# Kernel tuning notes

Measured on AMD Instinct MI355X. Metric: run time of the kernel, lower is better.

Reference implementation:

```python
import jax, jax.numpy as jnp
import numpy as np

B_SZ = 64            # oft_block_size
IN_F = 4096
OUT_F = 4096
R_IN = IN_F // B_SZ   # 64 blocks
R_OUT = OUT_F // B_SZ # 64 blocks
N_TRI = B_SZ * (B_SZ - 1) // 2  # 2016 packed strict-upper entries
NUM_NEUMANN = 5

_rows, _cols = np.triu_indices(B_SZ, k=1)
ROWS = jnp.asarray(_rows, dtype=jnp.int32)
COLS = jnp.asarray(_cols, dtype=jnp.int32)


def setup_inputs() -> dict:
    key = jax.random.key(0)
    k = jax.random.split(key, 5)
    x = jax.random.normal(k[0], (4, 2048, IN_F), dtype=jnp.float32)
    # small skew entries so the Neumann series approximates the Cayley transform
    Ro = jax.random.normal(k[1], (R_OUT, N_TRI), dtype=jnp.float32) * 0.01
    Ri = jax.random.normal(k[2], (R_IN, N_TRI), dtype=jnp.float32) * 0.01
    W = jax.random.normal(k[3], (OUT_F, IN_F), dtype=jnp.float32) * (1.0 / np.sqrt(IN_F))
    bias = jax.random.normal(k[4], (OUT_F,), dtype=jnp.float32) * 0.01
    rng = np.random.default_rng(0)
    perm_in = rng.permutation(IN_F)
    perm_in_inv = np.argsort(perm_in)
    perm_out = rng.permutation(OUT_F)
    return {
        "x": x, "Ro": Ro, "Ri": Ri, "W": W, "bias": bias,
        "perm_in_inv": jnp.asarray(perm_in_inv, dtype=jnp.int32),
        "perm_out": jnp.asarray(perm_out, dtype=jnp.int32),
    }


def _skew(vec):
    # vec: (r, n_tri) packed strict-upper entries -> (r, b, b) skew-symmetric
    r = vec.shape[0]
    M = jnp.zeros((r, B_SZ, B_SZ), dtype=vec.dtype).at[:, ROWS, COLS].set(vec)
    return M - jnp.swapaxes(M, -2, -1)


def _cayley_neumann(Q):
    # R = I + 2*(Q + Q^2 + Q^3 + Q^4)   (num_neumann_terms = 5)
    I = jnp.eye(B_SZ, dtype=Q.dtype)
    acc = Q
    Qp = Q
    for _ in range(3, NUM_NEUMANN):
        pass
    Q2 = jnp.matmul(Q, Q)
    acc = acc + Q2
    Qp = Q2
    for _ in range(3, NUM_NEUMANN):
        Qp = jnp.matmul(Qp, Q)
        acc = acc + Qp
    return I + 2.0 * acc


def reference(x, Ro, Ri, W, bias, perm_in_inv, perm_out):
    R_out = _cayley_neumann(_skew(Ro))   # (r_out, b, b)
    R_in = _cayley_neumann(_skew(Ri))    # (r_in, b, b)

    B, S, _ = x.shape
    xp = x[..., perm_in_inv]                               # input permutation
    xb = xp.reshape(B, S, R_IN, B_SZ)
    xR = jnp.einsum('bsrc,rcd->bsrd', xb, R_in)            # block-diag right rotate
    y = xR.reshape(B, S, IN_F) @ W.T + bias                # base linear
    yb = y.reshape(B, S, R_OUT, B_SZ)
    yR = jnp.einsum('bsrc,rcd->bsrd', yb, R_out)           # block-diag output rotate
    out = yR.reshape(B, S, OUT_F)[..., perm_out]           # output permutation
    return out
```

## Files before the change

### kernel.cpp

```cpp
#include <hip/hip_runtime.h>
#include <stdint.h>

#define IN_F 4096
#define OUT_F 4096
#define NTRI 2016

typedef unsigned short u16;
typedef __attribute__((ext_vector_type(8))) short short8;
typedef __attribute__((ext_vector_type(4))) float f32x4;
typedef __attribute__((ext_vector_type(4))) int i32x4;
typedef __attribute__((ext_vector_type(4))) unsigned short u16x4;

__device__ __forceinline__ u16 f2bf(float f) {
    uint32_t u = __builtin_bit_cast(uint32_t, f);
    u = (u + 0x7FFFu + ((u >> 16) & 1u)) >> 16;
    return (u16)u;
}

__device__ __forceinline__ void gload16(const void* g, void* l) {
    __builtin_amdgcn_global_load_lds((__attribute__((address_space(1))) void*)g,
                                     (__attribute__((address_space(3))) void*)l,
                                     16, 0, 0);
}

__global__ void k_inv_perm(const int* __restrict__ perm_out, int* __restrict__ pinv_out) {
    int i = blockIdx.x * 256 + threadIdx.x;
    if (i < OUT_F) pinv_out[perm_out[i]] = i;
}

__global__ __launch_bounds__(256) void k_cayley(const float* __restrict__ Ro,
                                                const float* __restrict__ Ri,
                                                float* __restrict__ Rout,
                                                u16* __restrict__ QT16,
                                                u16* __restrict__ P16) {
    __shared__ __align__(16) float Qs[64 * 64];
    __shared__ __align__(16) float Ps[64 * 68];
    __shared__ __align__(16) float Ts[64 * 68];
    int b = blockIdx.x;
    const float* vec = (b < 64) ? (Ro + (size_t)b * NTRI) : (Ri + (size_t)(b - 64) * NTRI);
    int t = threadIdx.x;
    int tr = t >> 4, tc = t & 15;
#pragma unroll
    for (int e = 0; e < 16; ++e) {
        int el = e * 256 + t;
        int i = el >> 6, j = el & 63;
        float q = 0.f;
        if (i < j) q =  vec[i * 63 - (i * (i - 1)) / 2 + (j - i - 1)];
        if (i > j) q = -vec[j * 63 - (j * (j - 1)) / 2 + (i - j - 1)];
        Qs[el] = q;
    }
    __syncthreads();
    float a2[4][4], a3[4][4], a4[4][4];
#pragma unroll
    for (int i = 0; i < 4; ++i)
#pragma unroll
        for (int j = 0; j < 4; ++j) { a2[i][j] = 0.f; a3[i][j] = 0.f; a4[i][j] = 0.f; }
    for (int k = 0; k < 64; ++k) {
        f32x4 qa = *(const f32x4*)&Qs[k * 64 + tr * 4];
        f32x4 qb = *(const f32x4*)&Qs[k * 64 + tc * 4];
#pragma unroll
        for (int i = 0; i < 4; ++i)
#pragma unroll
            for (int j = 0; j < 4; ++j) a2[i][j] -= qa[i] * qb[j];
    }
#pragma unroll
    for (int i = 0; i < 4; ++i)
#pragma unroll
        for (int j = 0; j < 4; ++j) Ps[(tr * 4 + i) * 68 + tc * 4 + j] = a2[i][j];
    __syncthreads();
    for (int k = 0; k < 64; ++k) {
        f32x4 pa = *(const f32x4*)&Ps[k * 68 + tr * 4];
        f32x4 qb = *(const f32x4*)&Qs[k * 64 + tc * 4];
#pragma unroll
        for (int i = 0; i < 4; ++i)
#pragma unroll
            for (int j = 0; j < 4; ++j) a3[i][j] += pa[i] * qb[j];
    }
#pragma unroll
    for (int i = 0; i < 4; ++i)
#pragma unroll
        for (int j = 0; j < 4; ++j) Ts[(tc * 4 + j) * 68 + tr * 4 + i] = -a3[i][j];
    __syncthreads();
    for (int k = 0; k < 64; ++k) {
        f32x4 ta = *(const f32x4*)&Ts[k * 68 + tr * 4];
        f32x4 qb = *(const f32x4*)&Qs[k * 64 + tc * 4];
#pragma unroll
        for (int i = 0; i < 4; ++i)
#pragma unroll
            for (int j = 0; j < 4; ++j) a4[i][j] -= ta[i] * qb[j];
    }
    if (b < 64) {
        float* dst = Rout + (size_t)b * 4096;
        u16* qt = QT16 + (size_t)b * 4096;
#pragma unroll
        for (int i = 0; i < 4; ++i) {
            int gi = tr * 4 + i;
            f32x4 q4 = *(const f32x4*)&Qs[gi * 64 + tc * 4];
            f32x4 o;
#pragma unroll
            for (int j = 0; j < 4; ++j) {
                int gj = tc * 4 + j;
                o[j] = 2.f * (q4[j] + a2[i][j] + a3[i][j] + a4[i][j]) + ((gi == gj) ? 1.f : 0.f);
            }
            *(f32x4*)&dst[gi * 64 + tc * 4] = o;
#pragma unroll
            for (int j = 0; j < 4; ++j) qt[(tc * 4 + j) * 64 + gi] = f2bf(o[j]);
        }
    } else {
        u16* p = P16 + (size_t)(b - 64) * 4096;
#pragma unroll
        for (int i = 0; i < 4; ++i) {
            int gi = tr * 4 + i;
            f32x4 q4 = *(const f32x4*)&Qs[gi * 64 + tc * 4];
            u16x4 pk;
#pragma unroll
            for (int j = 0; j < 4; ++j) {
                int gj = tc * 4 + j;
                float v = 2.f * (q4[j] + a2[i][j] + a3[i][j] + a4[i][j]) + ((gi == gj) ? 1.f : 0.f);
                pk[j] = f2bf(v);
            }
            *(u16x4*)&p[gi * 64 + tc * 4] = pk;
        }
    }
}

__global__ void k_bias(const float* __restrict__ bias, const float* __restrict__ Rout,
                       const int* __restrict__ perm_out, float* __restrict__ bfinal) {
    int j = blockIdx.x * 256 + threadIdx.x;
    if (j >= OUT_F) return;
    int o = perm_out[j];
    int r = o >> 6, d = o & 63;
    const float* Rb = Rout + (size_t)r * 4096;
    const float* bb = bias + r * 64;
    float s = 0.f;
    for (int c = 0; c < 64; ++c) s += bb[c] * Rb[c * 64 + d];
    bfinal[j] = s;
}

__global__ __launch_bounds__(256) void k_fold(const float* __restrict__ W,
                                              const u16* __restrict__ P16,
                                              const u16* __restrict__ QT16,
                                              const int* __restrict__ pinv_out,
                                              u16* __restrict__ Ctp) {
    __shared__ __align__(16) u16 Wst[128 * 64];
    __shared__ __align__(16) u16 Ut[64 * 128];
    const int s = blockIdx.x;
    const int br = blockIdx.y;
    const int t = threadIdx.x;
    const int lane = t & 63;
    const int w = t >> 6;
    const int fl = lane & 15;
    const int kg = lane >> 4;

    short8 bfP[4][2];
    const u16* Pbase = P16 + (size_t)s * 4096;
#pragma unroll
    for (int nf = 0; nf < 4; ++nf)
#pragma unroll
        for (int kk = 0; kk < 2; ++kk)
            bfP[nf][kk] = *(const short8*)(Pbase + (nf * 16 + fl) * 64 + kk * 32 + kg * 8);

#pragma unroll
    for (int q = 0; q < 4; ++q) {
        int ci = q * 256 + t;
        int row = ci >> 3, slot = ci & 7;
        const float* src = W + (size_t)(br * 128 + row) * IN_F + s * 64 + slot * 8;
        f32x4 v0 = *(const f32x4*)src;
        f32x4 v1 = *(const f32x4*)(src + 4);
        union { short8 v; u16 e[8]; } cv;
        cv.e[0] = f2bf(v0[0]); cv.e[1] = f2bf(v0[1]); cv.e[2] = f2bf(v0[2]); cv.e[3] = f2bf(v0[3]);
        cv.e[4] = f2bf(v1[0]); cv.e[5] = f2bf(v1[1]); cv.e[6] = f2bf(v1[2]); cv.e[7] = f2bf(v1[3]);
        *(short8*)&Wst[row * 64 + (slot ^ (row & 7)) * 8] = cv.v;
    }
    __syncthreads();

    f32x4 acc1[2][4];
#pragma unroll
    for (int mf = 0; mf < 2; ++mf)
#pragma unroll
        for (int nf = 0; nf < 4; ++nf) acc1[mf][nf] = f32x4{0.f, 0.f, 0.f, 0.f};
#pragma unroll
    for (int mf = 0; mf < 2; ++mf) {
        int row = w * 32 + mf * 16 + fl;
#pragma unroll
        for (int kk = 0; kk < 2; ++kk) {
            short8 a = *(const short8*)&Wst[row * 64 + ((kk * 4 + kg) ^ (row & 7)) * 8];
#pragma unroll
            for (int nf = 0; nf < 4; ++nf)
                acc1[mf][nf] = __builtin_amdgcn_mfma_f32_16x16x32_bf16(a, bfP[nf][kk], acc1[mf][nf], 0, 0, 0);
        }
    }
#pragma unroll
    for (int mf = 0; mf < 2; ++mf)
#pragma unroll
        for (int nf = 0; nf < 4; ++nf) {
            int i = nf * 16 + fl;
            int c = w * 32 + mf * 16 + kg * 4;
            u16x4 pk;
#pragma unroll
            for (int reg = 0; reg < 4; ++reg) pk[reg] = f2bf(acc1[mf][nf][reg]);
            int slot = c >> 3, half = (c >> 2) & 1;
            *(u16x4*)&Ut[i * 128 + ((slot ^ (i & 7)) << 3) + (half << 2)] = pk;
        }
    __syncthreads();

    const int rbl = w >> 1;
    const int r_g = br * 2 + rbl;
    short8 aQ[2][2];
#pragma unroll
    for (int mf2 = 0; mf2 < 2; ++mf2) {
        int d = (w & 1) * 32 + mf2 * 16 + fl;
#pragma unroll
        for (int kk = 0; kk < 2; ++kk)
            aQ[mf2][kk] = *(const short8*)(QT16 + (size_t)r_g * 4096 + d * 64 + kk * 32 + kg * 8);
    }
    f32x4 acc2[2][4];
#pragma unroll
    for (int mf2 = 0; mf2 < 2; ++mf2)
#pragma unroll
        for (int nf = 0; nf < 4; ++nf) acc2[mf2][nf] = f32x4{0.f, 0.f, 0.f, 0.f};
#pragma unroll
    for (int kk = 0; kk < 2; ++kk)
#pragma unroll
        for (int nf = 0; nf < 4; ++nf) {
            int i = nf * 16 + fl;
            int slot = rbl * 8 + kk * 4 + kg;
            short8 bu = *(const short8*)&Ut[i * 128 + ((slot ^ (i & 7)) << 3)];
#pragma unroll
            for (int mf2 = 0; mf2 < 2; ++mf2)
                acc2[mf2][nf] = __builtin_amdgcn_mfma_f32_16x16x32_bf16(aQ[mf2][kk], bu, acc2[mf2][nf], 0, 0, 0);
        }
#pragma unroll
    for (int mf2 = 0; mf2 < 2; ++mf2)
#pragma unroll
        for (int reg = 0; reg < 4; ++reg) {
            int o_g = br * 128 + w * 32 + mf2 * 16 + kg * 4 + reg;
            int j = pinv_out[o_g];
            u16* dst = Ctp + (size_t)j * IN_F + s * 64;
#pragma unroll
            for (int nf = 0; nf < 4; ++nf)
                dst[nf * 16 + fl] = f2bf(acc2[mf2][nf][reg]);
        }
}

__global__ __launch_bounds__(512) void k_xcast_perm(const float* __restrict__ x,
                                                    const int* __restrict__ pii,
                                                    u16* __restrict__ xb) {
    __shared__ __align__(16) float xr[4096];
    const int t = threadIdx.x;
    int pv[8];
    *(i32x4*)&pv[0] = *(const i32x4*)&pii[t * 8];
    *(i32x4*)&pv[4] = *(const i32x4*)&pii[t * 8 + 4];
    for (int r = 0; r < 8; ++r) {
        size_t s = (size_t)blockIdx.x * 8 + r;
        const float* src = x + s * 4096;
        *(f32x4*)&xr[t * 4]        = *(const f32x4*)&src[t * 4];
        *(f32x4*)&xr[2048 + t * 4] = *(const f32x4*)&src[2048 + t * 4];
        __syncthreads();
        union { short8 v; u16 e[8]; } o;
#pragma unroll
        for (int j = 0; j < 8; ++j) o.e[j] = f2bf(xr[pv[j]]);
        *(short8*)&xb[s * 4096 + t * 8] = o.v;
        __syncthreads();
    }
}

__global__ __launch_bounds__(512, 2) void k_gemm(const u16* __restrict__ A,
                                                 const u16* __restrict__ Bt,
                                                 const float* __restrict__ bias,
                                                 float* __restrict__ out) {
    __shared__ __align__(16) u16 lds[81920];
    const int t = threadIdx.x;
    const int lane = t & 63;
    const int wid = t >> 6;
    const int wr = wid >> 2, wc = wid & 3;

    int flat = blockIdx.y * gridDim.x + blockIdx.x;
    int swz  = (flat & 7) * 64 + (flat >> 3);
    int bm = swz >> 4;
    int bn = swz & 15;

    const int srow = t >> 2;
    const int sks  = (t & 3) ^ ((t >> 3) & 3);
    const u16* sA0 = A  + (size_t)(bm * 256 + srow) * IN_F + sks * 8;
    const u16* sA1 = sA0 + (size_t)128 * IN_F;
    const u16* sB0 = Bt + (size_t)(bn * 256 + srow) * IN_F + sks * 8;
    const u16* sB1 = sB0 + (size_t)128 * IN_F;
    u16* dA = lds + t * 8;
    u16* dB = lds + 8192 + t * 8;

    const int frow = lane & 15;
    const int kg = lane >> 4;
    const int swzr = kg ^ ((frow >> 1) & 3);
    const int aoff = (wr * 128 + frow) * 32 + swzr * 8;
    const int boff = 8192 + (wc * 64 + frow) * 32 + swzr * 8;

    f32x4 acc[8][4];
#pragma unroll
    for (int m = 0; m < 8; ++m)
#pragma unroll
        for (int n = 0; n < 4; ++n) acc[m][n] = f32x4{0.f, 0.f, 0.f, 0.f};

#pragma unroll
    for (int p = 0; p < 3; ++p) {
        int off = p * 32;
        int bb = p * 16384;
        gload16(sA0 + off, dA + bb); gload16(sA1 + off, dA + bb + 4096);
        gload16(sB0 + off, dB + bb); gload16(sB1 + off, dB + bb + 4096);
    }
    asm volatile("s_waitcnt vmcnt(4)" ::: "memory");
    __builtin_amdgcn_s_barrier();

    int b0 = 0;
    for (int p = 0; p < 64; ++p) {
        const int kt = 2 * p;
        int b1 = b0 + 1; if (b1 >= 5) b1 -= 5;
        int s0 = b0 + 3; if (s0 >= 5) s0 -= 5;
        int s1 = b0 + 4; if (s1 >= 5) s1 -= 5;
        {
            const u16* pa = lds + b0 * 16384 + aoff;
            const u16* pb = lds + b0 * 16384 + boff;
            short8 af[8], bf[4];
#pragma unroll
            for (int m = 0; m < 8; ++m) af[m] = *(const short8*)(pa + m * 512);
#pragma unroll
            for (int n = 0; n < 4; ++n) bf[n] = *(const short8*)(pb + n * 512);
            int ts = kt + 3;
            int off = (ts < 128 ? ts : 124) * 32;
            int bb = s0 * 16384;
            gload16(sA0 + off, dA + bb); gload16(sA1 + off, dA + bb + 4096);
            gload16(sB0 + off, dB + bb); gload16(sB1 + off, dB + bb + 4096);
            __builtin_amdgcn_s_setprio(1);
#pragma unroll
            for (int m = 0; m < 8; ++m)
#pragma unroll
                for (int n = 0; n < 4; ++n)
                    acc[m][n] = __builtin_amdgcn_mfma_f32_16x16x32_bf16(af[m], bf[n], acc[m][n], 0, 0, 0);
            __builtin_amdgcn_s_setprio(0);
        }
        {
            const u16* pa = lds + b1 * 16384 + aoff;
            const u16* pb = lds + b1 * 16384 + boff;
            short8 af[8], bf[4];
#pragma unroll
            for (int m = 0; m < 8; ++m) af[m] = *(const short8*)(pa + m * 512);
#pragma unroll
            for (int n = 0; n < 4; ++n) bf[n] = *(const short8*)(pb + n * 512);
            int ts = kt + 4;
            int off = (ts < 128 ? ts : 124) * 32;
            int bb = s1 * 16384;
            gload16(sA0 + off, dA + bb); gload16(sA1 + off, dA + bb + 4096);
            gload16(sB0 + off, dB + bb); gload16(sB1 + off, dB + bb + 4096);
            __builtin_amdgcn_s_setprio(1);
#pragma unroll
            for (int m = 0; m < 8; ++m)
#pragma unroll
                for (int n = 0; n < 4; ++n)
                    acc[m][n] = __builtin_amdgcn_mfma_f32_16x16x32_bf16(af[m], bf[n], acc[m][n], 0, 0, 0);
            __builtin_amdgcn_s_setprio(0);
        }
        asm volatile("s_waitcnt vmcnt(4)" ::: "memory");
        __builtin_amdgcn_s_barrier();
        b0 += 2; if (b0 >= 5) b0 -= 5;
    }
    asm volatile("s_waitcnt vmcnt(0)" ::: "memory");

    const int col0 = bn * 256 + wc * 64 + frow;
    const int row0 = bm * 256 + wr * 128 + kg * 4;
    float bv[4];
#pragma unroll
    for (int n = 0; n < 4; ++n) bv[n] = bias[col0 + n * 16];
#pragma unroll
    for (int m = 0; m < 8; ++m)
#pragma unroll
        for (int n = 0; n < 4; ++n)
#pragma unroll
            for (int i = 0; i < 4; ++i)
                out[(size_t)(row0 + m * 16 + i) * OUT_F + col0 + n * 16] = acc[m][n][i] + bv[n];
}

extern "C" void kernel_launch(void* const* d_in, const int* in_sizes, int n_in,
                              void* d_out, int out_size, void* d_ws, size_t ws_size,
                              hipStream_t stream) {
    (void)in_sizes; (void)n_in; (void)out_size; (void)ws_size;
    const float* x    = (const float*)d_in[0];
    const float* Ro   = (const float*)d_in[1];
    const float* Ri   = (const float*)d_in[2];
    const float* W    = (const float*)d_in[3];
    const float* bias = (const float*)d_in[4];
    const int* perm_in_inv = (const int*)d_in[5];
    const int* perm_out    = (const int*)d_in[6];
    float* out = (float*)d_out;

    char* ws = (char*)d_ws;
    float* Rout   = (float*)(ws);
    u16*   P16    = (u16*)(ws + (1ull << 20));
    u16*   QT16   = (u16*)(ws + (1ull << 20) + (1 << 19));
    int*   pinvo  = (int*)(ws + (2ull << 20));
    float* bfinal = (float*)(ws + (2ull << 20) + (1 << 16));
    u16*   Ctp    = (u16*)(ws + (4ull << 20));
    u16*   xb     = (u16*)(ws + (36ull << 20));

    k_inv_perm<<<16, 256, 0, stream>>>(perm_out, pinvo);
    k_cayley<<<128, 256, 0, stream>>>(Ro, Ri, Rout, QT16, P16);
    k_bias<<<16, 256, 0, stream>>>(bias, Rout, perm_out, bfinal);
    k_fold<<<dim3(64, 32), 256, 0, stream>>>(W, P16, QT16, pinvo, Ctp);
    k_xcast_perm<<<1024, 512, 0, stream>>>(x, perm_in_inv, xb);
    k_gemm<<<dim3(16, 32), 512, 0, stream>>>(xb, Ctp, bfinal, out);
}
```

Measured before the change: 335.2 us.

## Restructure GEMM main loop into quadrant-interleaved double-buffered schedule with K=64 tiles

Replaces the 5-stage ring of K=32 LDS tiles with two K=64 buffers, using an 8-way XOR swizzle. Each K tile is split into four MFMA quadrants, and global-to-LDS loads for half-tiles are issued between them with barriers, an HipKittens-style 8-wave ping-pong schedule. The goal is to overlap LDS reads, global loads and MFMA work more finely and to cut LDS usage. In exchange it adds many more barriers per iteration and leaves less prefetch depth.

```diff
diff --git a/kernel.cpp b/kernel.cpp
--- a/kernel.cpp
+++ b/kernel.cpp
@@ -22,6 +22,8 @@
                                      (__attribute__((address_space(3))) void*)l,
                                      16, 0, 0);
 }
+
+#define FENCE() asm volatile("" ::: "memory")
 
 __global__ void k_inv_perm(const int* __restrict__ perm_out, int* __restrict__ pinv_out) {
     int i = blockIdx.x * 256 + threadIdx.x;
@@ -269,7 +271,7 @@
                                                  const u16* __restrict__ Bt,
                                                  const float* __restrict__ bias,
                                                  float* __restrict__ out) {
-    __shared__ __align__(16) u16 lds[81920];
+    __shared__ __align__(16) u16 lds[65536];
     const int t = threadIdx.x;
     const int lane = t & 63;
     const int wid = t >> 6;
@@ -280,20 +282,43 @@
     int bm = swz >> 4;
     int bn = swz & 15;
 
-    const int srow = t >> 2;
-    const int sks  = (t & 3) ^ ((t >> 3) & 3);
-    const u16* sA0 = A  + (size_t)(bm * 256 + srow) * IN_F + sks * 8;
-    const u16* sA1 = sA0 + (size_t)128 * IN_F;
-    const u16* sB0 = Bt + (size_t)(bn * 256 + srow) * IN_F + sks * 8;
-    const u16* sB1 = sB0 + (size_t)128 * IN_F;
-    u16* dA = lds + t * 8;
-    u16* dB = lds + 8192 + t * 8;
+    const int sk = ((t & 7) ^ ((t >> 3) & 7)) * 8;
+    const u16* gA = A  + (size_t)(bm * 256 + (t >> 3)) * IN_F + sk;
+    const u16* gB = Bt + (size_t)(bn * 256 + (t >> 3)) * IN_F + sk;
+    u16* ldst = lds + t * 8;
+
+#define STAGE_A(buf, r0, kt) do { \
+        u16* d_ = ldst + (buf) * 32768 + (r0) * 64; \
+        const u16* s_ = gA + (size_t)(r0) * IN_F + (kt) * 64; \
+        gload16(s_, d_); gload16(s_ + (size_t)64 * IN_F, d_ + 4096); } while (0)
+#define STAGE_B(buf, r0, kt) do { \
+        u16* d_ = ldst + (buf) * 32768 + 16384 + (r0) * 64; \
+        const u16* s_ = gB + (size_t)(r0) * IN_F + (kt) * 64; \
+        gload16(s_, d_); gload16(s_ + (size_t)64 * IN_F, d_ + 4096); } while (0)
 
     const int frow = lane & 15;
     const int kg = lane >> 4;
-    const int swzr = kg ^ ((frow >> 1) & 3);
-    const int aoff = (wr * 128 + frow) * 32 + swzr * 8;
-    const int boff = 8192 + (wc * 64 + frow) * 32 + swzr * 8;
+    int fswz[2];
+    fswz[0] = ((0 * 4 + kg) ^ (frow & 7)) * 8;
+    fswz[1] = ((1 * 4 + kg) ^ (frow & 7)) * 8;
+    const int arow = (wr * 128 + frow) * 64;
+    const int brow = 16384 + (wc * 64 + frow) * 64;
+
+#define LDA(B, M, KS) (*(const short8*)(lds + (B) + arow + (M) * 1024 + fswz[KS]))
+#define LDB(B, N, KS) (*(const short8*)(lds + (B) + brow + (N) * 1024 + fswz[KS]))
+
+#define MQ(AR, BR, MB, NB) do { \
+        __builtin_amdgcn_s_setprio(1); \
+        _Pragma("unroll") for (int ks_ = 0; ks_ < 2; ++ks_) \
+        _Pragma("unroll") for (int m_ = 0; m_ < 4; ++m_) \
+        _Pragma("unroll") for (int n_ = 0; n_ < 2; ++n_) \
+            acc[(MB) + m_][(NB) + n_] = __builtin_amdgcn_mfma_f32_16x16x32_bf16( \
+                AR[m_][ks_], BR[n_][ks_], acc[(MB) + m_][(NB) + n_], 0, 0, 0); \
+        __builtin_amdgcn_s_setprio(0); } while (0)
+
+#define BAR_LG() do { FENCE(); __builtin_amdgcn_s_barrier(); \
+        asm volatile("s_waitcnt lgkmcnt(0)" ::: "memory"); } while (0)
+#define BAR() do { FENCE(); __builtin_amdgcn_s_barrier(); FENCE(); } while (0)
 
     f32x4 acc[8][4];
 #pragma unroll
@@ -301,67 +326,86 @@
 #pragma unroll
         for (int n = 0; n < 4; ++n) acc[m][n] = f32x4{0.f, 0.f, 0.f, 0.f};
 
-#pragma unroll
-    for (int p = 0; p < 3; ++p) {
-        int off = p * 32;
-        int bb = p * 16384;
-        gload16(sA0 + off, dA + bb); gload16(sA1 + off, dA + bb + 4096);
-        gload16(sB0 + off, dB + bb); gload16(sB1 + off, dB + bb + 4096);
-    }
+    STAGE_A(0, 0, 0); STAGE_A(0, 128, 0);
+    STAGE_B(0, 0, 0); STAGE_B(0, 128, 0);
+    STAGE_B(1, 0, 1); STAGE_A(1, 0, 1);
     asm volatile("s_waitcnt vmcnt(4)" ::: "memory");
     __builtin_amdgcn_s_barrier();
-
-    int b0 = 0;
-    for (int p = 0; p < 64; ++p) {
-        const int kt = 2 * p;
-        int b1 = b0 + 1; if (b1 >= 5) b1 -= 5;
-        int s0 = b0 + 3; if (s0 >= 5) s0 -= 5;
-        int s1 = b0 + 4; if (s1 >= 5) s1 -= 5;
-        {
-            const u16* pa = lds + b0 * 16384 + aoff;
-            const u16* pb = lds + b0 * 16384 + boff;
-            short8 af[8], bf[4];
-#pragma unroll
-            for (int m = 0; m < 8; ++m) af[m] = *(const short8*)(pa + m * 512);
-#pragma unroll
-            for (int n = 0; n < 4; ++n) bf[n] = *(const short8*)(pb + n * 512);
-            int ts = kt + 3;
-            int off = (ts < 128 ? ts : 124) * 32;
-            int bb = s0 * 16384;
-            gload16(sA0 + off, dA + bb); gload16(sA1 + off, dA + bb + 4096);
-            gload16(sB0 + off, dB + bb); gload16(sB1 + off, dB + bb + 4096);
-            __builtin_amdgcn_s_setprio(1);
-#pragma unroll
-            for (int m = 0; m < 8; ++m)
-#pragma unroll
-                for (int n = 0; n < 4; ++n)
-                    acc[m][n] = __builtin_amdgcn_mfma_f32_16x16x32_bf16(af[m], bf[n], acc[m][n], 0, 0, 0);
-            __builtin_amdgcn_s_setprio(0);
-        }
-        {
-            const u16* pa = lds + b1 * 16384 + aoff;
-            const u16* pb = lds + b1 * 16384 + boff;
-            short8 af[8], bf[4];
-#pragma unroll
-            for (int m = 0; m < 8; ++m) af[m] = *(const short8*)(pa + m * 512);
-#pragma unroll
-            for (int n = 0; n < 4; ++n) bf[n] = *(const short8*)(pb + n * 512);
-            int ts = kt + 4;
-            int off = (ts < 128 ? ts : 124) * 32;
-            int bb = s1 * 16384;
-            gload16(sA0 + off, dA + bb); gload16(sA1 + off, dA + bb + 4096);
-            gload16(sB0 + off, dB + bb); gload16(sB1 + off, dB + bb + 4096);
-            __builtin_amdgcn_s_setprio(1);
-#pragma unroll
-            for (int m = 0; m < 8; ++m)
-#pragma unroll
-                for (int n = 0; n < 4; ++n)
-                    acc[m][n] = __builtin_amdgcn_mfma_f32_16x16x32_bf16(af[m], bf[n], acc[m][n], 0, 0, 0);
-            __builtin_amdgcn_s_setprio(0);
-        }
+    FENCE();
+
+    short8 alo[4][2], ahi[4][2], blo[2][2], bhi[2][2];
+
+    for (int i = 0; i < 32; ++i) {
+        const int kt1 = 2 * i + 1;
+        const int kn0 = (i < 31) ? 2 * i + 2 : 62;
+        const int kn1 = (i < 31) ? 2 * i + 3 : 63;
+
+#pragma unroll
+        for (int m = 0; m < 4; ++m)
+#pragma unroll
+            for (int ks = 0; ks < 2; ++ks) alo[m][ks] = LDA(0, m, ks);
+#pragma unroll
+        for (int n = 0; n < 2; ++n)
+#pragma unroll
+            for (int ks = 0; ks < 2; ++ks) blo[n][ks] = LDB(0, n, ks);
+        STAGE_A(1, 128, kt1);
+        BAR_LG();
+        MQ(alo, blo, 0, 0);
+        BAR();
+#pragma unroll
+        for (int n = 0; n < 2; ++n)
+#pragma unroll
+            for (int ks = 0; ks < 2; ++ks) bhi[n][ks] = LDB(0, 2 + n, ks);
+        STAGE_B(1, 128, kt1);
+        BAR_LG();
+        MQ(alo, bhi, 0, 2);
+        BAR();
+#pragma unroll
+        for (int m = 0; m < 4; ++m)
+#pragma unroll
+            for (int ks = 0; ks < 2; ++ks) ahi[m][ks] = LDA(0, 4 + m, ks);
+        STAGE_B(0, 0, kn0);
+        BAR_LG();
+        MQ(ahi, blo, 4, 0);
+        BAR();
+        STAGE_A(0, 0, kn0);
         asm volatile("s_waitcnt vmcnt(4)" ::: "memory");
-        __builtin_amdgcn_s_barrier();
-        b0 += 2; if (b0 >= 5) b0 -= 5;
+        BAR();
+        MQ(ahi, bhi, 4, 2);
+        BAR();
+#pragma unroll
+        for (int m = 0; m < 4; ++m)
+#pragma unroll
+            for (int ks = 0; ks < 2; ++ks) alo[m][ks] = LDA(32768, m, ks);
+#pragma unroll
+        for (int n = 0; n < 2; ++n)
+#pragma unroll
+            for (int ks = 0; ks < 2; ++ks) blo[n][ks] = LDB(32768, n, ks);
+        STAGE_A(0, 128, kn0);
+        BAR_LG();
+        MQ(alo, blo, 0, 0);
+        BAR();
+#pragma unroll
+        for (int n = 0; n < 2; ++n)
+#pragma unroll
+            for (int ks = 0; ks < 2; ++ks) bhi[n][ks] = LDB(32768, 2 + n, ks);
+        STAGE_B(0, 128, kn0);
+        BAR_LG();
+        MQ(alo, bhi, 0, 2);
+        BAR();
+#pragma unroll
+        for (int m = 0; m < 4; ++m)
+#pragma unroll
+            for (int ks = 0; ks < 2; ++ks) ahi[m][ks] = LDA(32768, 4 + m, ks);
+        STAGE_B(1, 0, kn1);
+        BAR_LG();
+        MQ(ahi, blo, 4, 0);
+        BAR();
+        STAGE_A(1, 0, kn1);
+        asm volatile("s_waitcnt vmcnt(4)" ::: "memory");
+        BAR();
+        MQ(ahi, bhi, 4, 2);
+        BAR();
     }
     asm volatile("s_waitcnt vmcnt(0)" ::: "memory");
 
@@ -377,6 +421,13 @@
 #pragma unroll
             for (int i = 0; i < 4; ++i)
                 out[(size_t)(row0 + m * 16 + i) * OUT_F + col0 + n * 16] = acc[m][n][i] + bv[n];
+#undef STAGE_A
+#undef STAGE_B
+#undef LDA
+#undef LDB
+#undef MQ
+#undef BAR_LG
+#undef BAR
 }
 
 extern "C" void kernel_launch(void* const* d_in, const int* in_sizes, int n_in,
```

After: 325.3 us. 2.9% less time.

## Merge prep kernels into two launches and switch GEMM to 4-stage ring pipeline

Applied to the files above, without the earlier changes.

Folds the inverse-permutation into the Cayley kernel and merges the weight fold, x cast/permute and bias kernels into one launch dispatched by block index, cutting launch count from six to three and letting independent stages share the GPU. The main GEMM LDS ring drops from 5 buffers to 4, going from two k-steps per barrier to one barrier per k-step with vmcnt(8). The smaller LDS footprint may improve occupancy, but the extra barriers and shallower wait window may expose more load latency.

```diff
diff --git a/kernel.cpp b/kernel.cpp
--- a/kernel.cpp
+++ b/kernel.cpp
@@ -23,22 +23,27 @@
                                      16, 0, 0);
 }
 
-__global__ void k_inv_perm(const int* __restrict__ perm_out, int* __restrict__ pinv_out) {
-    int i = blockIdx.x * 256 + threadIdx.x;
-    if (i < OUT_F) pinv_out[perm_out[i]] = i;
-}
-
-__global__ __launch_bounds__(256) void k_cayley(const float* __restrict__ Ro,
-                                                const float* __restrict__ Ri,
-                                                float* __restrict__ Rout,
-                                                u16* __restrict__ QT16,
-                                                u16* __restrict__ P16) {
+__global__ __launch_bounds__(256) void k_prep(const float* __restrict__ Ro,
+                                              const float* __restrict__ Ri,
+                                              const int* __restrict__ perm_out,
+                                              float* __restrict__ Rout,
+                                              u16* __restrict__ QT16,
+                                              u16* __restrict__ P16,
+                                              int* __restrict__ pinv_out) {
+    const int b = blockIdx.x;
+    const int t = threadIdx.x;
+    if (b == 128) {
+#pragma unroll
+        for (int e = 0; e < 16; ++e) {
+            int i = e * 256 + t;
+            pinv_out[perm_out[i]] = i;
+        }
+        return;
+    }
     __shared__ __align__(16) float Qs[64 * 64];
     __shared__ __align__(16) float Ps[64 * 68];
     __shared__ __align__(16) float Ts[64 * 68];
-    int b = blockIdx.x;
     const float* vec = (b < 64) ? (Ro + (size_t)b * NTRI) : (Ri + (size_t)(b - 64) * NTRI);
-    int t = threadIdx.x;
     int tr = t >> 4, tc = t & 15;
 #pragma unroll
     for (int e = 0; e < 16; ++e) {
@@ -124,144 +129,148 @@
     }
 }
 
-__global__ void k_bias(const float* __restrict__ bias, const float* __restrict__ Rout,
-                       const int* __restrict__ perm_out, float* __restrict__ bfinal) {
-    int j = blockIdx.x * 256 + threadIdx.x;
-    if (j >= OUT_F) return;
-    int o = perm_out[j];
-    int r = o >> 6, d = o & 63;
-    const float* Rb = Rout + (size_t)r * 4096;
-    const float* bb = bias + r * 64;
-    float s = 0.f;
-    for (int c = 0; c < 64; ++c) s += bb[c] * Rb[c * 64 + d];
-    bfinal[j] = s;
-}
-
-__global__ __launch_bounds__(256) void k_fold(const float* __restrict__ W,
+__global__ __launch_bounds__(256) void k_work(const float* __restrict__ W,
                                               const u16* __restrict__ P16,
                                               const u16* __restrict__ QT16,
                                               const int* __restrict__ pinv_out,
-                                              u16* __restrict__ Ctp) {
-    __shared__ __align__(16) u16 Wst[128 * 64];
-    __shared__ __align__(16) u16 Ut[64 * 128];
-    const int s = blockIdx.x;
-    const int br = blockIdx.y;
+                                              const float* __restrict__ x,
+                                              const int* __restrict__ pii,
+                                              const float* __restrict__ bias,
+                                              const float* __restrict__ Rout,
+                                              const int* __restrict__ perm_out,
+                                              u16* __restrict__ Ctp,
+                                              u16* __restrict__ xb,
+                                              float* __restrict__ bfinal) {
+    const int fb = blockIdx.x;
     const int t = threadIdx.x;
-    const int lane = t & 63;
-    const int w = t >> 6;
-    const int fl = lane & 15;
-    const int kg = lane >> 4;
-
-    short8 bfP[4][2];
-    const u16* Pbase = P16 + (size_t)s * 4096;
-#pragma unroll
-    for (int nf = 0; nf < 4; ++nf)
+    if (fb < 2048) {
+        __shared__ __align__(16) u16 Wst[128 * 64];
+        __shared__ __align__(16) u16 Ut[64 * 128];
+        const int s = fb & 63;
+        const int br = fb >> 6;
+        const int lane = t & 63;
+        const int w = t >> 6;
+        const int fl = lane & 15;
+        const int kg = lane >> 4;
+
+        short8 bfP[4][2];
+        const u16* Pbase = P16 + (size_t)s * 4096;
+#pragma unroll
+        for (int nf = 0; nf < 4; ++nf)
+#pragma unroll
+            for (int kk = 0; kk < 2; ++kk)
+                bfP[nf][kk] = *(const short8*)(Pbase + (nf * 16 + fl) * 64 + kk * 32 + kg * 8);
+
+#pragma unroll
+        for (int q = 0; q < 4; ++q) {
+            int ci = q * 256 + t;
+            int row = ci >> 3, slot = ci & 7;
+            const float* src = W + (size_t)(br * 128 + row) * IN_F + s * 64 + slot * 8;
+            f32x4 v0 = *(const f32x4*)src;
+            f32x4 v1 = *(const f32x4*)(src + 4);
+            union { short8 v; u16 e[8]; } cv;
+            cv.e[0] = f2bf(v0[0]); cv.e[1] = f2bf(v0[1]); cv.e[2] = f2bf(v0[2]); cv.e[3] = f2bf(v0[3]);
+            cv.e[4] = f2bf(v1[0]); cv.e[5] = f2bf(v1[1]); cv.e[6] = f2bf(v1[2]); cv.e[7] = f2bf(v1[3]);
+            *(short8*)&Wst[row * 64 + (slot ^ (row & 7)) * 8] = cv.v;
+        }
+        __syncthreads();
+
+        f32x4 acc1[2][4];
+#pragma unroll
+        for (int mf = 0; mf < 2; ++mf)
+#pragma unroll
+            for (int nf = 0; nf < 4; ++nf) acc1[mf][nf] = f32x4{0.f, 0.f, 0.f, 0.f};
+#pragma unroll
+        for (int mf = 0; mf < 2; ++mf) {
+            int row = w * 32 + mf * 16 + fl;
+#pragma unroll
+            for (int kk = 0; kk < 2; ++kk) {
+                short8 a = *(const short8*)&Wst[row * 64 + ((kk * 4 + kg) ^ (row & 7)) * 8];
+#pragma unroll
+                for (int nf = 0; nf < 4; ++nf)
+                    acc1[mf][nf] = __builtin_amdgcn_mfma_f32_16x16x32_bf16(a, bfP[nf][kk], acc1[mf][nf], 0, 0, 0);
+            }
+        }
+#pragma unroll
+        for (int mf = 0; mf < 2; ++mf)
+#pragma unroll
+            for (int nf = 0; nf < 4; ++nf) {
+                int i = nf * 16 + fl;
+                int c = w * 32 + mf * 16 + kg * 4;
+                u16x4 pk;
+#pragma unroll
+                for (int reg = 0; reg < 4; ++reg) pk[reg] = f2bf(acc1[mf][nf][reg]);
+                int slot = c >> 3, half = (c >> 2) & 1;
+                *(u16x4*)&Ut[i * 128 + ((slot ^ (i & 7)) << 3) + (half << 2)] = pk;
+            }
+        __syncthreads();
+
+        const int rbl = w >> 1;
+        const int r_g = br * 2 + rbl;
+        short8 aQ[2][2];
+#pragma unroll
+        for (int mf2 = 0; mf2 < 2; ++mf2) {
+            int d = (w & 1) * 32 + mf2 * 16 + fl;
+#pragma unroll
+            for (int kk = 0; kk < 2; ++kk)
+                aQ[mf2][kk] = *(const short8*)(QT16 + (size_t)r_g * 4096 + d * 64 + kk * 32 + kg * 8);
+        }
+        f32x4 acc2[2][4];
+#pragma unroll
+        for (int mf2 = 0; mf2 < 2; ++mf2)
+#pragma unroll
+            for (int nf = 0; nf < 4; ++nf) acc2[mf2][nf] = f32x4{0.f, 0.f, 0.f, 0.f};
 #pragma unroll
         for (int kk = 0; kk < 2; ++kk)
-            bfP[nf][kk] = *(const short8*)(Pbase + (nf * 16 + fl) * 64 + kk * 32 + kg * 8);
-
-#pragma unroll
-    for (int q = 0; q < 4; ++q) {
-        int ci = q * 256 + t;
-        int row = ci >> 3, slot = ci & 7;
-        const float* src = W + (size_t)(br * 128 + row) * IN_F + s * 64 + slot * 8;
-        f32x4 v0 = *(const f32x4*)src;
-        f32x4 v1 = *(const f32x4*)(src + 4);
-        union { short8 v; u16 e[8]; } cv;
-        cv.e[0] = f2bf(v0[0]); cv.e[1] = f2bf(v0[1]); cv.e[2] = f2bf(v0[2]); cv.e[3] = f2bf(v0[3]);
-        cv.e[4] = f2bf(v1[0]); cv.e[5] = f2bf(v1[1]); cv.e[6] = f2bf(v1[2]); cv.e[7] = f2bf(v1[3]);
-        *(short8*)&Wst[row * 64 + (slot ^ (row & 7)) * 8] = cv.v;
-    }
-    __syncthreads();
-
-    f32x4 acc1[2][4];
-#pragma unroll
-    for (int mf = 0; mf < 2; ++mf)
-#pragma unroll
-        for (int nf = 0; nf < 4; ++nf) acc1[mf][nf] = f32x4{0.f, 0.f, 0.f, 0.f};
-#pragma unroll
-    for (int mf = 0; mf < 2; ++mf) {
-        int row = w * 32 + mf * 16 + fl;
-#pragma unroll
-        for (int kk = 0; kk < 2; ++kk) {
-            short8 a = *(const short8*)&Wst[row * 64 + ((kk * 4 + kg) ^ (row & 7)) * 8];
-#pragma unroll
-            for (int nf = 0; nf < 4; ++nf)
-                acc1[mf][nf] = __builtin_amdgcn_mfma_f32_16x16x32_bf16(a, bfP[nf][kk], acc1[mf][nf], 0, 0, 0);
-        }
-    }
-#pragma unroll
-    for (int mf = 0; mf < 2; ++mf)
-#pragma unroll
-        for (int nf = 0; nf < 4; ++nf) {
-            int i = nf * 16 + fl;
-            int c = w * 32 + mf * 16 + kg * 4;
-            u16x4 pk;
-#pragma unroll
-            for (int reg = 0; reg < 4; ++reg) pk[reg] = f2bf(acc1[mf][nf][reg]);
-            int slot = c >> 3, half = (c >> 2) & 1;
-            *(u16x4*)&Ut[i * 128 + ((slot ^ (i & 7)) << 3) + (half << 2)] = pk;
-        }
-    __syncthreads();
-
-    const int rbl = w >> 1;
-    const int r_g = br * 2 + rbl;
-    short8 aQ[2][2];
-#pragma unroll
-    for (int mf2 = 0; mf2 < 2; ++mf2) {
-        int d = (w & 1) * 32 + mf2 * 16 + fl;
-#pragma unroll
-        for (int kk = 0; kk < 2; ++kk)
-            aQ[mf2][kk] = *(const short8*)(QT16 + (size_t)r_g * 4096 + d * 64 + kk * 32 + kg * 8);
-    }
-    f32x4 acc2[2][4];
-#pragma unroll
-    for (int mf2 = 0; mf2 < 2; ++mf2)
-#pragma unroll
-        for (int nf = 0; nf < 4; ++nf) acc2[mf2][nf] = f32x4{0.f, 0.f, 0.f, 0.f};
-#pragma unroll
-    for (int kk = 0; kk < 2; ++kk)
-#pragma unroll
-        for (int nf = 0; nf < 4; ++nf) {
-            int i = nf * 16 + fl;
-            int slot = rbl * 8 + kk * 4 + kg;
-            short8 bu = *(const short8*)&Ut[i * 128 + ((slot ^ (i & 7)) << 3)];
-#pragma unroll
-            for (int mf2 = 0; mf2 < 2; ++mf2)
-                acc2[mf2][nf] = __builtin_amdgcn_mfma_f32_16x16x32_bf16(aQ[mf2][kk], bu, acc2[mf2][nf], 0, 0, 0);
-        }
-#pragma unroll
-    for (int mf2 = 0; mf2 < 2; ++mf2)
-#pragma unroll
-        for (int reg = 0; reg < 4; ++reg) {
-            int o_g = br * 128 + w * 32 + mf2 * 16 + kg * 4 + reg;
-            int j = pinv_out[o_g];
-            u16* dst = Ctp + (size_t)j * IN_F + s * 64;
-#pragma unroll
-            for (int nf = 0; nf < 4; ++nf)
-                dst[nf * 16 + fl] = f2bf(acc2[mf2][nf][reg]);
-        }
-}
-
-__global__ __launch_bounds__(512) void k_xcast_perm(const float* __restrict__ x,
-                                                    const int* __restrict__ pii,
-                                                    u16* __restrict__ xb) {
-    __shared__ __align__(16) float xr[4096];
-    const int t = threadIdx.x;
-    int pv[8];
-    *(i32x4*)&pv[0] = *(const i32x4*)&pii[t * 8];
-    *(i32x4*)&pv[4] = *(const i32x4*)&pii[t * 8 + 4];
-    for (int r = 0; r < 8; ++r) {
-        size_t s = (size_t)blockIdx.x * 8 + r;
-        const float* src = x + s * 4096;
-        *(f32x4*)&xr[t * 4]        = *(const f32x4*)&src[t * 4];
-        *(f32x4*)&xr[2048 + t * 4] = *(const f32x4*)&src[2048 + t * 4];
-        __syncthreads();
-        union { short8 v; u16 e[8]; } o;
-#pragma unroll
-        for (int j = 0; j < 8; ++j) o.e[j] = f2bf(xr[pv[j]]);
-        *(short8*)&xb[s * 4096 + t * 8] = o.v;
-        __syncthreads();
+#pragma unroll
+            for (int nf = 0; nf < 4; ++nf) {
+                int i = nf * 16 + fl;
+                int slot = rbl * 8 + kk * 4 + kg;
+                short8 bu = *(const short8*)&Ut[i * 128 + ((slot ^ (i & 7)) << 3)];
+#pragma unroll
+                for (int mf2 = 0; mf2 < 2; ++mf2)
+                    acc2[mf2][nf] = __builtin_amdgcn_mfma_f32_16x16x32_bf16(aQ[mf2][kk], bu, acc2[mf2][nf], 0, 0, 0);
+            }
+#pragma unroll
+        for (int mf2 = 0; mf2 < 2; ++mf2)
+#pragma unroll
+            for (int reg = 0; reg < 4; ++reg) {
+                int o_g = br * 128 + w * 32 + mf2 * 16 + kg * 4 + reg;
+                int j = pinv_out[o_g];
+                u16* dst = Ctp + (size_t)j * IN_F + s * 64;
+#pragma unroll
+                for (int nf = 0; nf < 4; ++nf)
+                    dst[nf * 16 + fl] = f2bf(acc2[mf2][nf][reg]);
+            }
+    } else if (fb < 3072) {
+        __shared__ __align__(16) float xr[4096];
+        const int blk = fb - 2048;
+        int pv[16];
+#pragma unroll
+        for (int q = 0; q < 4; ++q) *(i32x4*)&pv[q * 4] = *(const i32x4*)&pii[t * 16 + q * 4];
+        for (int r = 0; r < 8; ++r) {
+            size_t srow = (size_t)blk * 8 + r;
+            const float* src = x + srow * 4096;
+#pragma unroll
+            for (int q = 0; q < 4; ++q)
+                *(f32x4*)&xr[q * 1024 + t * 4] = *(const f32x4*)&src[q * 1024 + t * 4];
+            __syncthreads();
+            union { short8 v; u16 e[8]; } o0, o1;
+#pragma unroll
+            for (int j = 0; j < 8; ++j) { o0.e[j] = f2bf(xr[pv[j]]); o1.e[j] = f2bf(xr[pv[8 + j]]); }
+            *(short8*)&xb[srow * 4096 + t * 16] = o0.v;
+            *(short8*)&xb[srow * 4096 + t * 16 + 8] = o1.v;
+            __syncthreads();
+        }
+    } else {
+        int j = (fb - 3072) * 256 + t;
+        int o = perm_out[j];
+        int r = o >> 6, d = o & 63;
+        const float* Rb = Rout + (size_t)r * 4096;
+        const float* bb = bias + r * 64;
+        float s = 0.f;
+        for (int c = 0; c < 64; ++c) s += bb[c] * Rb[c * 64 + d];
+        bfinal[j] = s;
     }
 }
 
@@ -269,7 +278,7 @@
                                                  const u16* __restrict__ Bt,
                                                  const float* __restrict__ bias,
                                                  float* __restrict__ out) {
-    __shared__ __align__(16) u16 lds[81920];
+    __shared__ __align__(16) u16 lds[65536];
     const int t = threadIdx.x;
     const int lane = t & 63;
     const int wid = t >> 6;
@@ -308,28 +317,29 @@
         gload16(sA0 + off, dA + bb); gload16(sA1 + off, dA + bb + 4096);
         gload16(sB0 + off, dB + bb); gload16(sB1 + off, dB + bb + 4096);
     }
-    asm volatile("s_waitcnt vmcnt(4)" ::: "memory");
+    asm volatile("s_waitcnt vmcnt(8)" ::: "memory");
     __builtin_amdgcn_s_barrier();
 
-    int b0 = 0;
-    for (int p = 0; p < 64; ++p) {
-        const int kt = 2 * p;
-        int b1 = b0 + 1; if (b1 >= 5) b1 -= 5;
-        int s0 = b0 + 3; if (s0 >= 5) s0 -= 5;
-        int s1 = b0 + 4; if (s1 >= 5) s1 -= 5;
-        {
-            const u16* pa = lds + b0 * 16384 + aoff;
-            const u16* pb = lds + b0 * 16384 + boff;
+    for (int t4 = 0; t4 < 128; t4 += 4) {
+#pragma unroll
+        for (int u = 0; u < 4; ++u) {
+            const int kt = t4 + u;
+            const u16* base = lds + u * 16384;
             short8 af[8], bf[4];
+            const u16* pa = base + aoff;
+            const u16* pb = base + boff;
 #pragma unroll
             for (int m = 0; m < 8; ++m) af[m] = *(const short8*)(pa + m * 512);
 #pragma unroll
             for (int n = 0; n < 4; ++n) bf[n] = *(const short8*)(pb + n * 512);
-            int ts = kt + 3;
-            int off = (ts < 128 ? ts : 124) * 32;
-            int bb = s0 * 16384;
-            gload16(sA0 + off, dA + bb); gload16(sA1 + off, dA + bb + 4096);
-            gload16(sB0 + off, dB + bb); gload16(sB1 + off, dB + bb + 4096);
+            {
+                int ts = kt + 3;
+                int tsc = ts < 128 ? ts : 124;
+                int off = tsc * 32;
+                int bb = ((kt + 3) & 3) * 16384;
+                gload16(sA0 + off, dA + bb); gload16(sA1 + off, dA + bb + 4096);
+                gload16(sB0 + off, dB + bb); gload16(sB1 + off, dB + bb + 4096);
+            }
             __builtin_amdgcn_s_setprio(1);
 #pragma unroll
             for (int m = 0; m < 8; ++m)
@@ -337,31 +347,9 @@
                 for (int n = 0; n < 4; ++n)
                     acc[m][n] = __builtin_amdgcn_mfma_f32_16x16x32_bf16(af[m], bf[n], acc[m][n], 0, 0, 0);
             __builtin_amdgcn_s_setprio(0);
-        }
-        {
-            const u16* pa = lds + b1 * 16384 + aoff;
-            const u16* pb = lds + b1 * 16384 + boff;
-            short8 af[8], bf[4];
-#pragma unroll
-            for (int m = 0; m < 8; ++m) af[m] = *(const short8*)(pa + m * 512);
-#pragma unroll
-            for (int n = 0; n < 4; ++n) bf[n] = *(const short8*)(pb + n * 512);
-            int ts = kt + 4;
-            int off = (ts < 128 ? ts : 124) * 32;
-            int bb = s1 * 16384;
-            gload16(sA0 + off, dA + bb); gload16(sA1 + off, dA + bb + 4096);
-            gload16(sB0 + off, dB + bb); gload16(sB1 + off, dB + bb + 4096);
-            __builtin_amdgcn_s_setprio(1);
-#pragma unroll
-            for (int m = 0; m < 8; ++m)
-#pragma unroll
-                for (int n = 0; n < 4; ++n)
-                    acc[m][n] = __builtin_amdgcn_mfma_f32_16x16x32_bf16(af[m], bf[n], acc[m][n], 0, 0, 0);
-            __builtin_amdgcn_s_setprio(0);
-        }
-        asm volatile("s_waitcnt vmcnt(4)" ::: "memory");
-        __builtin_amdgcn_s_barrier();
-        b0 += 2; if (b0 >= 5) b0 -= 5;
+            asm volatile("s_waitcnt vmcnt(8)" ::: "memory");
+            __builtin_amdgcn_s_barrier();
+        }
     }
     asm volatile("s_waitcnt vmcnt(0)" ::: "memory");
 
@@ -401,10 +389,8 @@
     u16*   Ctp    = (u16*)(ws + (4ull << 20));
     u16*   xb     = (u16*)(ws + (36ull << 20));
 
-    k_inv_perm<<<16, 256, 0, stream>>>(perm_out, pinvo);
-    k_cayley<<<128, 256, 0, stream>>>(Ro, Ri, Rout, QT16, P16);
-    k_bias<<<16, 256, 0, stream>>>(bias, Rout, perm_out, bfinal);
-    k_fold<<<dim3(64, 32), 256, 0, stream>>>(W, P16, QT16, pinvo, Ctp);
-    k_xcast_perm<<<1024, 512, 0, stream>>>(x, perm_in_inv, xb);
+    k_prep<<<129, 256, 0, stream>>>(Ro, Ri, perm_out, Rout, QT16, P16, pinvo);
+    k_work<<<3088, 256, 0, stream>>>(W, P16, QT16, pinvo, x, perm_in_inv, bias, Rout,
+                                     perm_out, Ctp, xb, bfinal);
     k_gemm<<<dim3(16, 32), 512, 0, stream>>>(xb, Ctp, bfinal, out);
 }
```

New measurement: 318.2 us. 5.1% less time.
